# Performance work log

Measured on AMD Instinct MI355X. Metric: run time of the kernel, lower is better.

## Reference

```python
import jax, jax.numpy as jnp
import numpy as np

# B docs, N total nodes (E entities + M mentions + S sentences), R relation types, H heads
B, N, E, M, S, D, IN, R, H = 8, 224, 64, 128, 32, 256, 300, 5, 4


def setup_inputs() -> dict:
    key = jax.random.key(0)
    ks = jax.random.split(key, 24)
    p = lambda k, shp: jax.random.normal(k, shp, dtype=jnp.float32) * 0.05
    return {
        "nodes": jax.random.normal(ks[0], (B, N, IN), dtype=jnp.float32),
        "adj": (jax.random.uniform(ks[1], (B, R, N, N)) < 0.05).astype(jnp.float32),
        "mentions": jax.random.normal(ks[2], (B, M, D), dtype=jnp.float32),
        "sentences": jax.random.normal(ks[3], (B * S, D), dtype=jnp.float32),
        "Wr0": p(ks[4], (R, IN, D)), "br0": p(ks[5], (R, D)),
        "Wr1": p(ks[6], (R, D, D)), "br1": p(ks[7], (R, D)),
        "W00": p(ks[8], (IN, D)), "b00": p(ks[9], (D,)),
        "W01": p(ks[10], (D, D)), "b01": p(ks[11], (D,)),
        "Wq_h": p(ks[12], (D, D)), "Wk_h": p(ks[13], (D, D)),
        "Wv_h": p(ks[14], (D, D)), "Wo_h": p(ks[15], (D, D)),
        "Wq_t": p(ks[16], (D, D)), "Wk_t": p(ks[17], (D, D)),
        "Wv_t": p(ks[18], (D, D)), "Wo_t": p(ks[19], (D, D)),
        # entity id (local, 0..E-1) of each mention: each entity owns M/E=2 mentions
        "info_eid": (jnp.arange(B * M, dtype=jnp.int32) % E).reshape(B, M),
        # flat sentence index of each mention, within its own doc's sentence block
        "info_sid": jax.random.randint(ks[20], (B, M), 0, S, dtype=jnp.int32)
        + jnp.arange(B, dtype=jnp.int32)[:, None] * S,
    }


def _mha(key_t, value_t, query_t, mask, Wq, Wk, Wv, Wo):
    # mask: [B, P, M], True = exclude (mention does not belong to the masked entity)
    b, p, d = query_t.shape
    m = key_t.shape[1]
    dk = d // H
    Q = (query_t @ Wq).reshape(b, p, H, dk)
    K = (key_t @ Wk).reshape(b, m, H, dk)
    V = (value_t @ Wv).reshape(b, m, H, dk)
    s = jnp.einsum("bphk,bmhk->bhpm", Q, K) / jnp.sqrt(jnp.asarray(dk, Q.dtype))
    s = jnp.where(mask[:, None, :, :], jnp.asarray(-1e9, s.dtype), s)
    a = jax.nn.softmax(s, axis=-1)
    ctx = jnp.einsum("bhpm,bmhk->bphk", a, V).reshape(b, p, d)
    return ctx @ Wo


def reference(nodes, adj, mentions, sentences, Wr0, br0, Wr1, br1, W00, b00,
              W01, b01, Wq_h, Wk_h, Wv_h, Wo_h, Wq_t, Wk_t, Wv_t, Wo_t,
              info_eid, info_sid):
    # ---- RGCN_Layer: per-relation message passing, degree-normalized ----
    # denom: in-degree per node summed over relations, +1 (matches torch.sparse.sum dim=1)
    denoms = adj.sum(axis=3).sum(axis=1)[..., None] + 1.0  # [B, N, 1]

    def rgcn_layer(x, Wr, br, W0, b0):
        xW = jnp.einsum("bni,rid->brnd", x, Wr) + br[None, :, None, :]  # [B,R,N,D]
        AxW = jnp.einsum("brnm,brmd->bnd", adj, xW)  # aggregate + sum over relations
        return jax.nn.relu((AxW + x @ W0 + b0) / denoms)

    h = rgcn_layer(nodes, Wr0, br0, W00, b00)
    gcn_out = rgcn_layer(h, Wr1, br1, W01, b01)  # [B, N, D] global node reps

    # ---- Local_rep_layer: masked pairwise multi-head attention ----
    ents = gcn_out[:, :E, :]  # query='global': entities = global nodes (first E rows)
    # pair (i, j): query_1 -> entity i, query_2 -> entity j
    q1 = jnp.broadcast_to(ents[:, :, None, :], (B, E, E, D)).reshape(B, E * E, D)
    q2 = jnp.broadcast_to(ents[:, None, :, :], (B, E, E, D)).reshape(B, E * E, D)
    mention_sen_rep = sentences[info_sid]  # F.embedding(info[:,4], sentences) -> [B,M,D]
    # index_m[b, e, m] True iff mention m does NOT belong to entity e
    index_m = info_eid[:, None, :] != jnp.arange(E, dtype=info_eid.dtype)[None, :, None]
    mask_h = jnp.broadcast_to(index_m[:, :, None, :], (B, E, E, M)).reshape(B, E * E, M)
    mask_t = jnp.broadcast_to(index_m[:, None, :, :], (B, E, E, M)).reshape(B, E * E, M)
    rep_h = _mha(mention_sen_rep, mentions, q2, mask_h, Wq_h, Wk_h, Wv_h, Wo_h)
    rep_t = _mha(mention_sen_rep, mentions, q1, mask_t, Wq_t, Wk_t, Wv_t, Wo_t)
    # concatenate outputs along node axis for a single return array
    return jnp.concatenate([gcn_out, rep_h, rep_t], axis=1)  # [B, N + 2*E*E, D]
```

## Files before the change

### kernel.cpp

```cpp
#include <hip/hip_runtime.h>
#include <math.h>

#define B_ 8
#define N_ 224
#define E_ 64
#define M_ 128
#define S_ 32
#define D_ 256
#define IN_ 300
#define R_ 5
#define H_ 4
#define DK_ 64
#define OUTROWS (N_ + 2 * E_ * E_)
#define CAP_ 192
#define BN_ (B_ * N_)

typedef __attribute__((ext_vector_type(8))) short bf16x8;
typedef __attribute__((ext_vector_type(8))) unsigned short u16x8;
typedef __attribute__((ext_vector_type(4))) float f32x4;

__device__ inline short f2bf(float f) {
    union { float f; unsigned u; } x; x.f = f;
    unsigned u = x.u;
    unsigned r = (u + 0x7fffu + ((u >> 16) & 1u)) >> 16;
    return (short)r;
}
__device__ inline float bf2f(unsigned short s) {
    union { unsigned u; float f; } x; x.u = ((unsigned)s) << 16; return x.f;
}

__device__ inline void gload16(const void* g, void* l) {
    __builtin_amdgcn_global_load_lds(
        (const __attribute__((address_space(1))) unsigned int*)g,
        (__attribute__((address_space(3))) unsigned int*)l, 16, 0, 0);
}

#define PRE_PACK 1376
#define PRE_EDGE (PRE_PACK + BN_)
#define PRE_ML   (PRE_EDGE + 2)
#define CVT_N    573440
#define CVT_M    262144
#define PRE_TOT  (PRE_ML + 1072)

__global__ __launch_bounds__(256) void mega_pre(
    short* __restrict__ Wb,
    const float* Wr0, const float* W00, const float* Wr1, const float* W01,
    const float* Wkh, const float* Wkt, const float* Wvh, const float* Wvt,
    const float* Wqh, const float* Wqt, const float* Woh, const float* Wot,
    const float* __restrict__ adj, int* __restrict__ ecnt, int* __restrict__ elist,
    float* __restrict__ evals, float* __restrict__ den,
    const int* __restrict__ eid, int* __restrict__ mcnt, int* __restrict__ mlist,
    const float* __restrict__ nodes, const float* __restrict__ mentions,
    const float* __restrict__ sentences, const int* __restrict__ sid,
    short* __restrict__ nodesb, short* __restrict__ mentb, short* __restrict__ msrb) {
    __shared__ int smemi[528];
    __shared__ int wtot[4];
    __shared__ float wsum[4];
    int blk = blockIdx.x, tid = threadIdx.x;

    if (blk < PRE_PACK) {
        short (*T)[33] = (short(*)[33])smemi;
        int t = blk;
        const float* src; short* outp; int outld, klim, n0, k0;
        if (t < 480) {
            int z = t / 80, tt = t % 80;
            n0 = (tt & 7) * 32; k0 = (tt >> 3) * 32;
            outp = Wb + (size_t)z * 81920; outld = 320; klim = IN_;
            src = (z < 5) ? Wr0 + (size_t)z * IN_ * D_ : W00;
        } else if (t < 864) {
            int l = t - 480, z = l / 64, tt = l % 64;
            n0 = (tt & 7) * 32; k0 = (tt >> 3) * 32;
            outp = Wb + 491520 + (size_t)z * 65536; outld = 256; klim = 256;
            src = (z < 5) ? Wr1 + (size_t)z * D_ * D_ : W01;
        } else if (t < 992) {
            int l = t - 864, z = l / 64, tt = l % 64;
            n0 = (tt & 7) * 32; k0 = (tt >> 3) * 32;
            outp = Wb + 884736 + (size_t)z * 65536; outld = 256; klim = 256;
            src = z ? Wkt : Wkh;
        } else if (t < 1120) {
            int l = t - 992, z = l / 64, tt = l % 64;
            n0 = (tt & 7) * 32; k0 = (tt >> 3) * 32;
            outp = Wb + 1146880 + (size_t)z * 65536; outld = 256; klim = 256;
            src = z ? Wvt : Wvh;
        } else if (t < 1248) {
            int l = t - 1120, z = l / 64, tt = l % 64;
            n0 = (tt & 7) * 32; k0 = (tt >> 3) * 32;
            outp = Wb + 1409024 + (size_t)z * 65536; outld = 256; klim = 256;
            src = z ? Wqt : Wqh;
        } else {
            int l = t - 1248, z = l / 16, tt = l % 16;
            n0 = (tt & 7) * 32; k0 = (tt >> 3) * 32;
            outp = Wb + 1671168 + (size_t)z * 16384; outld = 64; klim = 64;
            int which = z >> 2, h = z & 3;
            src = (which ? Wot : Woh) + (size_t)(h * 64) * D_;
        }
        int tx = tid & 31, ty = tid >> 5;
#pragma unroll
        for (int i = 0; i < 4; ++i) {
            int k = k0 + ty + 8 * i;
            float v = (k < klim) ? src[(size_t)k * D_ + n0 + tx] : 0.f;
            T[tx][ty + 8 * i] = f2bf(v);
        }
        __syncthreads();
#pragma unroll
        for (int i = 0; i < 4; ++i) {
            int n = ty + 8 * i;
            outp[(size_t)(n0 + n) * outld + k0 + tx] = T[n][tx];
        }
    } else if (blk < PRE_EDGE) {
        int local = blk - PRE_PACK;
        int bn = (local & 7) * N_ + (local >> 3);
        int b = bn / N_, n = bn % N_;
        int lane = tid & 63, wv4 = tid >> 6;
        int idxs[5]; float vals[5];
        int cloc = 0; float sloc = 0.f;
        for (int e = tid; e < R_ * N_; e += 256) {
            int r = e / N_, m = e % N_;
            float v = adj[(((size_t)(b * R_ + r)) * N_ + n) * N_ + m];
            if (v != 0.f) { idxs[cloc] = r * BN_ + m; vals[cloc] = v; ++cloc; sloc += v; }
        }
        int v = cloc;
#pragma unroll
        for (int st = 1; st < 64; st <<= 1) {
            int o = __shfl_up(v, st, 64);
            if (lane >= st) v += o;
        }
        float fs = sloc;
#pragma unroll
        for (int st = 32; st > 0; st >>= 1) fs += __shfl_xor(fs, st, 64);
        if (lane == 63) wtot[wv4] = v;
        if (lane == 0)  wsum[wv4] = fs;
        __syncthreads();
        int woff = 0;
        for (int i = 0; i < wv4; ++i) woff += wtot[i];
        int off = woff + v - cloc;
        int total = wtot[0] + wtot[1] + wtot[2] + wtot[3];
        size_t base = (size_t)bn * CAP_;
        for (int i = 0; i < cloc; ++i) {
            int p = off + i;
            if (p < CAP_) { elist[base + p] = idxs[i]; evals[base + p] = vals[i]; }
        }
        if (tid == 0) {
            ecnt[bn] = total < CAP_ ? total : CAP_;
            den[bn] = wsum[0] + wsum[1] + wsum[2] + wsum[3] + 1.0f;
        }
    } else if (blk < PRE_ML) {
        int t = (blk - PRE_EDGE) * 256 + tid;
        if (t < B_ * E_) {
            int b = t / E_, i = t % E_;
            int c = 0;
            for (int m = 0; m < M_; ++m)
                if (eid[b * M_ + m] == i) mlist[(size_t)t * M_ + c++] = m;
            mcnt[t] = c;
        }
    } else {
        int idx = (blk - PRE_ML) * 1024 + tid * 4;
#pragma unroll
        for (int j = 0; j < 4; ++j) {
            int i = idx + j;
            if (i < CVT_N) {
                int row = i / 320, k = i % 320;
                nodesb[i] = (k < IN_) ? f2bf(nodes[(size_t)row * IN_ + k]) : (short)0;
            } else if (i < CVT_N + CVT_M) {
                int i2 = i - CVT_N;
                mentb[i2] = f2bf(mentions[i2]);
            } else {
                int i3 = i - CVT_N - CVT_M;
                int bm = i3 >> 8, d = i3 & 255;
                msrb[i3] = f2bf(sentences[(size_t)sid[bm] * D_ + d]);
            }
        }
    }
}

__global__ __launch_bounds__(256) void axw_gather(
    const short* __restrict__ xWb,
    const int* __restrict__ ecnt, const int* __restrict__ elist,
    const float* __restrict__ evals, const float* __restrict__ den,
    short* __restrict__ hb, float* __restrict__ out, long long out_bstride,
    short* __restrict__ entsb) {
    int bid = blockIdx.x;
    int bn = (bid & 7) * N_ + (bid >> 3);
    int b = bn / N_, n = bn % N_;
    int tid = threadIdx.x, wv = tid >> 6, dq = tid & 63;
    int c = ecnt[bn];
    int bno = b * N_;
    const int* lst = elist + (size_t)bn * CAP_;
    const float* vls = evals + (size_t)bn * CAP_;
    float4 acc = make_float4(0.f, 0.f, 0.f, 0.f);
#pragma unroll 2
    for (int k = wv; k < c; k += 4) {
        int rm = lst[k];
        float v = vls[k];
        ushort4 x4 = *(const ushort4*)&xWb[((size_t)(rm + bno)) * 256 + dq * 4];
        acc.x += v * bf2f(x4.x); acc.y += v * bf2f(x4.y);
        acc.z += v * bf2f(x4.z); acc.w += v * bf2f(x4.w);
    }
    __shared__ float4 red[4][64];
    red[wv][dq] = acc;
    __syncthreads();
    if (tid < 64) {
        float4 s0 = red[0][dq], s1 = red[1][dq], s2 = red[2][dq], s3 = red[3][dq];
        ushort4 t4 = *(const ushort4*)&xWb[((size_t)(5 * BN_ + bn)) * 256 + dq * 4];
        float inv = 1.f / den[bn];
        float4 o;
        o.x = fmaxf((s0.x + s1.x + s2.x + s3.x + bf2f(t4.x)) * inv, 0.f);
        o.y = fmaxf((s0.y + s1.y + s2.y + s3.y + bf2f(t4.y)) * inv, 0.f);
        o.z = fmaxf((s0.z + s1.z + s2.z + s3.z + bf2f(t4.z)) * inv, 0.f);
        o.w = fmaxf((s0.w + s1.w + s2.w + s3.w + bf2f(t4.w)) * inv, 0.f);
        if (hb) {
            ushort4 hw = { (unsigned short)f2bf(o.x), (unsigned short)f2bf(o.y),
                           (unsigned short)f2bf(o.z), (unsigned short)f2bf(o.w) };
            *(ushort4*)&hb[(size_t)bn * 256 + dq * 4] = hw;
        }
        if (out)
            *(float4*)&out[(size_t)b * out_bstride + (size_t)n * 256 + dq * 4] = o;
        if (entsb && n < E_) {
            ushort4 ew = { (unsigned short)f2bf(o.x), (unsigned short)f2bf(o.y),
                           (unsigned short)f2bf(o.z), (unsigned short)f2bf(o.w) };
            *(ushort4*)&entsb[((size_t)b * E_ + n) * 256 + dq * 4] = ew;
        }
    }
}

struct GDesc {
    const short* A; const short* Bt; short* C; const float* bias;
    int lda, ldbk, ldc, Kloop, ny;
};
struct GTable { GDesc d[14]; };

__global__ __launch_bounds__(256) void gemm_multi(GTable T) {
    GDesc g = T.d[blockIdx.z];
    if ((int)blockIdx.y >= g.ny) return;

    __shared__ short As[64 * 64];
    __shared__ short Bs[64 * 64];
    int tid = threadIdx.x;
    int lane = tid & 63, wv = tid >> 6;
    int wr = wv >> 1, wc = wv & 1;
    int fr = lane & 15;
    int so = lane >> 4;
    int row0 = blockIdx.y * 64, col0 = blockIdx.x * 64;

    int l8 = lane >> 3;
    int sl = (lane & 7) ^ l8;
    int c0 = 2 * wv, c1 = c0 + 1;
    int ra0 = row0 + 8 * c0 + l8, ra1 = row0 + 8 * c1 + l8;
    int rb0 = col0 + 8 * c0 + l8, rb1 = col0 + 8 * c1 + l8;

    f32x4 acc00 = {0.f,0.f,0.f,0.f}, acc01 = acc00, acc10 = acc00, acc11 = acc00;

    int rA0 = wr * 32 + fr, rA1 = rA0 + 16;
    int rB0 = wc * 32 + fr, rB1 = rB0 + 16;
    int sw = fr & 7;

    for (int k0 = 0; k0 < g.Kloop; k0 += 64) {
        gload16(&g.A [(size_t)ra0 * g.lda  + k0 + sl * 8], &As[c0 * 512]);
        gload16(&g.A [(size_t)ra1 * g.lda  + k0 + sl * 8], &As[c1 * 512]);
        gload16(&g.Bt[(size_t)rb0 * g.ldbk + k0 + sl * 8], &Bs[c0 * 512]);
        gload16(&g.Bt[(size_t)rb1 * g.ldbk + k0 + sl * 8], &Bs[c1 * 512]);
        __syncthreads();
#pragma unroll
        for (int ks = 0; ks < 2; ++ks) {
            int s = ks * 4 + so;
            bf16x8 a0 = *(bf16x8*)&As[rA0 * 64 + ((s ^ sw) << 3)];
            bf16x8 a1 = *(bf16x8*)&As[rA1 * 64 + ((s ^ sw) << 3)];
            bf16x8 b0 = *(bf16x8*)&Bs[rB0 * 64 + ((s ^ sw) << 3)];
            bf16x8 b1 = *(bf16x8*)&Bs[rB1 * 64 + ((s ^ sw) << 3)];
            acc00 = __builtin_amdgcn_mfma_f32_16x16x32_bf16(a0, b0, acc00, 0, 0, 0);
            acc01 = __builtin_amdgcn_mfma_f32_16x16x32_bf16(a0, b1, acc01, 0, 0, 0);
            acc10 = __builtin_amdgcn_mfma_f32_16x16x32_bf16(a1, b0, acc10, 0, 0, 0);
            acc11 = __builtin_amdgcn_mfma_f32_16x16x32_bf16(a1, b1, acc11, 0, 0, 0);
        }
        __syncthreads();
    }

    int rbase = row0 + wr * 32 + (lane >> 4) * 4;
    int cbase = col0 + wc * 32 + fr;
    f32x4 accs[2][2] = {{acc00, acc01}, {acc10, acc11}};
#pragma unroll
    for (int mi = 0; mi < 2; ++mi) {
#pragma unroll
        for (int nj = 0; nj < 2; ++nj) {
            int cc = cbase + nj * 16;
            float bval = g.bias ? g.bias[cc] : 0.f;
#pragma unroll
            for (int r = 0; r < 4; ++r) {
                int cr = rbase + mi * 16 + r;
                g.C[(size_t)cr * g.ldc + cc] = f2bf(accs[mi][nj][r] + bval);
            }
        }
    }
}

__device__ inline float dot64_bf(const short* q, const short* k) {
    float dot = 0.f;
#pragma unroll
    for (int t8 = 0; t8 < 8; ++t8) {
        u16x8 qv = *(const u16x8*)(q + t8 * 8);
        u16x8 kv = *(const u16x8*)(k + t8 * 8);
#pragma unroll
        for (int j = 0; j < 8; ++j) dot += bf2f(qv[j]) * bf2f(kv[j]);
    }
    return dot;
}

__global__ __launch_bounds__(256) void combine_kernel(
    const short* __restrict__ Qb, const short* __restrict__ Kb,
    const short* __restrict__ VWb, const int* __restrict__ cnt,
    const int* __restrict__ mlist, float* __restrict__ out) {
    int bid = blockIdx.x;
    int g = bid & 15, me = bid >> 4;
    int b = g & 7, z = g >> 3;
    const short* Q  = Qb  + (size_t)z * (B_ * E_ * D_);
    const short* K  = Kb  + (size_t)z * (B_ * M_ * D_);
    const short* VW = VWb + (size_t)z * (B_ * M_ * H_ * D_);
    int baserow = N_ + z * (E_ * E_);
    int tid = threadIdx.x;
    int dq = tid & 63;
    __shared__ float sVW[2][H_ * D_];
    __shared__ float sS[E_][H_][2];
    int c = cnt[b * E_ + me];
    const int* lst = mlist + (size_t)(b * E_ + me) * M_;

    if (c >= 1 && c <= 2) {
        for (int k = 0; k < c; ++k) {
            ushort4 v4 = *(const ushort4*)(VW + ((size_t)b * M_ + lst[k]) * (H_ * D_) + tid * 4);
            *(float4*)&sVW[k][tid * 4] =
                make_float4(bf2f(v4.x), bf2f(v4.y), bf2f(v4.z), bf2f(v4.w));
        }
        for (int e = tid; e < E_ * H_ * 2; e += 256) {
            int k = e & 1, hh = (e >> 1) & 3, ql = e >> 3;
            if (k < c) {
                const short* Qrow = Q + ((size_t)b * E_ + ql) * D_ + hh * DK_;
                const short* Krow = K + ((size_t)b * M_ + lst[k]) * D_ + hh * DK_;
                sS[ql][hh][k] = dot64_bf(Qrow, Krow) * 0.125f;
            }
        }
        __syncthreads();
        {
            int hh = tid & 3, ql = tid >> 2;
            float mx = sS[ql][hh][0];
            for (int k = 1; k < c; ++k) mx = fmaxf(mx, sS[ql][hh][k]);
            float w[2]; float sm = 0.f;
            for (int k = 0; k < c; ++k) { w[k] = __expf(sS[ql][hh][k] - mx); sm += w[k]; }
            float inv = 1.f / sm;
            for (int k = 0; k < c; ++k) sS[ql][hh][k] = w[k] * inv;
        }
        __syncthreads();
        for (int qq = tid >> 6; qq < E_; qq += 4) {
            float4 acc = make_float4(0.f, 0.f, 0.f, 0.f);
#pragma unroll
            for (int hh = 0; hh < H_; ++hh)
                for (int k = 0; k < c; ++k) {
                    float w = sS[qq][hh][k];
                    float4 v = *(const float4*)&sVW[k][hh * D_ + dq * 4];
                    acc.x += w * v.x; acc.y += w * v.y; acc.z += w * v.z; acc.w += w * v.w;
                }
            int row = z ? (qq * E_ + me) : (me * E_ + qq);
            *(float4*)&out[((size_t)b * OUTROWS + baserow + row) * D_ + dq * 4] = acc;
        }
    } else if (c == 0) {
        float s = 0.f;
        for (int m = 0; m < M_; ++m)
            for (int hh = 0; hh < H_; ++hh)
                s += bf2f((unsigned short)VW[((size_t)b * M_ + m) * (H_ * D_) + hh * D_ + tid]);
        sVW[0][tid] = s * (1.0f / M_);
        __syncthreads();
        for (int qq = tid >> 6; qq < E_; qq += 4) {
            float4 v = *(const float4*)&sVW[0][dq * 4];
            int row = z ? (qq * E_ + me) : (me * E_ + qq);
            *(float4*)&out[((size_t)b * OUTROWS + baserow + row) * D_ + dq * 4] = v;
        }
    } else {
        {
            int hh = tid & 3, ql = tid >> 2;
            const short* Qrow = Q + ((size_t)b * E_ + ql) * D_ + hh * DK_;
            float mx = -1e30f;
            for (int k = 0; k < c; ++k) {
                const short* Krow = K + ((size_t)b * M_ + lst[k]) * D_ + hh * DK_;
                mx = fmaxf(mx, dot64_bf(Qrow, Krow) * 0.125f);
            }
            float sm = 0.f;
            for (int k = 0; k < c; ++k) {
                const short* Krow = K + ((size_t)b * M_ + lst[k]) * D_ + hh * DK_;
                sm += __expf(dot64_bf(Qrow, Krow) * 0.125f - mx);
            }
            sS[ql][hh][0] = mx;
            sS[ql][hh][1] = sm;
        }
        __syncthreads();
        for (int qq = tid >> 6; qq < E_; qq += 4) {
            float4 acc = make_float4(0.f, 0.f, 0.f, 0.f);
            for (int hh = 0; hh < H_; ++hh) {
                float mx = sS[qq][hh][0], inv = 1.f / sS[qq][hh][1];
                const short* Qrow = Q + ((size_t)b * E_ + qq) * D_ + hh * DK_;
                for (int k = 0; k < c; ++k) {
                    const short* Krow = K + ((size_t)b * M_ + lst[k]) * D_ + hh * DK_;
                    float w = __expf(dot64_bf(Qrow, Krow) * 0.125f - mx) * inv;
                    ushort4 v4 = *(const ushort4*)(VW + ((size_t)b * M_ + lst[k]) * (H_ * D_) + hh * D_ + dq * 4);
                    acc.x += w * bf2f(v4.x); acc.y += w * bf2f(v4.y);
                    acc.z += w * bf2f(v4.z); acc.w += w * bf2f(v4.w);
                }
            }
            int row = z ? (qq * E_ + me) : (me * E_ + qq);
            *(float4*)&out[((size_t)b * OUTROWS + baserow + row) * D_ + dq * 4] = acc;
        }
    }
}

extern "C" void kernel_launch(void* const* d_in, const int* in_sizes, int n_in,
                              void* d_out, int out_size, void* d_ws, size_t ws_size,
                              hipStream_t stream) {
    const float* nodes     = (const float*)d_in[0];
    const float* adj       = (const float*)d_in[1];
    const float* mentions  = (const float*)d_in[2];
    const float* sentences = (const float*)d_in[3];
    const float* Wr0 = (const float*)d_in[4];
    const float* br0 = (const float*)d_in[5];
    const float* Wr1 = (const float*)d_in[6];
    const float* br1 = (const float*)d_in[7];
    const float* W00 = (const float*)d_in[8];
    const float* b00 = (const float*)d_in[9];
    const float* W01 = (const float*)d_in[10];
    const float* b01 = (const float*)d_in[11];
    const float* Wq_h = (const float*)d_in[12];
    const float* Wk_h = (const float*)d_in[13];
    const float* Wv_h = (const float*)d_in[14];
    const float* Wo_h = (const float*)d_in[15];
    const float* Wq_t = (const float*)d_in[16];
    const float* Wk_t = (const float*)d_in[17];
    const float* Wv_t = (const float*)d_in[18];
    const float* Wo_t = (const float*)d_in[19];
    const int* info_eid = (const int*)d_in[20];
    const int* info_sid = (const int*)d_in[21];
    float* out  = (float*)d_out;
    float* pool = (float*)d_ws;

    short* xWb   = (short*)pool;
    short* hb    = (short*)(pool + 1376256);
    short* entsb = (short*)(pool + 1605632);
    short* KVb   = (short*)(pool + 1671168);
    short* nodesb= (short*)(pool + 2195456);
    short* msrb  = (short*)(pool + 2482176);
    short* mentb = (short*)(pool + 2613248);
    short* Wb    = (short*)(pool + 2744320);
    int*   elist = (int*)(pool + 3645440);
    float* evals = pool + 3989504;
    int*   ecnt  = (int*)(pool + 4333568);
    float* den   = pool + 4335360;
    int*   mcnt  = (int*)(pool + 4337152);
    int*   mlist = (int*)(pool + 4337664);
    short* VWb   = (short*)(pool + 4403200);
    short* Qb    = (short*)(pool + 5451776);

    short* W1t = Wb;
    short* W2t = Wb + 491520;
    short* WKt = Wb + 884736;
    short* WVt = Wb + 1146880;
    short* WQt = Wb + 1409024;
    short* WOt = Wb + 1671168;

    mega_pre<<<PRE_TOT, 256, 0, stream>>>(
        Wb, Wr0, W00, Wr1, W01, Wk_h, Wk_t, Wv_h, Wv_t, Wq_h, Wq_t, Wo_h, Wo_t,
        adj, ecnt, elist, evals, den, info_eid, mcnt, mlist,
        nodes, mentions, sentences, info_sid, nodesb, mentb, msrb);

    {
        GTable T = {};
        for (int z = 0; z < 6; ++z)
            T.d[z] = { nodesb, W1t + z * 81920, xWb + (size_t)z * BN_ * D_,
                       (z < 5) ? br0 + z * D_ : b00, 320, 320, D_, 320, 28 };
        for (int zp = 0; zp < 4; ++zp) {
            int half = zp >> 1, wt = zp & 1;
            T.d[6 + zp] = { msrb + half * 262144, (half ? WVt : WKt) + wt * 65536,
                            KVb + half * 524288 + wt * 262144,
                            nullptr, D_, D_, D_, D_, 16 };
        }
        gemm_multi<<<dim3(4, 28, 10), 256, 0, stream>>>(T);
    }
    axw_gather<<<BN_, 256, 0, stream>>>(xWb, ecnt, elist, evals, den,
                                        hb, nullptr, 0, nullptr);
    {
        GTable T = {};
        for (int z = 0; z < 6; ++z)
            T.d[z] = { hb, W2t + z * 65536, xWb + (size_t)z * BN_ * D_,
                       (z < 5) ? br1 + z * D_ : b01, D_, D_, D_, D_, 28 };
        for (int zp = 0; zp < 8; ++zp) {
            int which = zp >> 2, hh = zp & 3;
            T.d[6 + zp] = { KVb + 524288 + which * 262144 + hh * DK_,
                            WOt + which * 65536 + hh * 16384,
                            VWb + (size_t)which * (B_ * M_ * H_ * D_) + hh * D_,
                            nullptr, D_, DK_, H_ * D_, DK_, 16 };
        }
        gemm_multi<<<dim3(4, 28, 14), 256, 0, stream>>>(T);
    }
    axw_gather<<<BN_, 256, 0, stream>>>(xWb, ecnt, elist, evals, den,
                                        nullptr, out, (long long)OUTROWS * D_, entsb);
    {
        GTable T = {};
        for (int which = 0; which < 2; ++which)
            T.d[which] = { entsb, WQt + which * 65536, Qb + which * 131072,
                           nullptr, D_, D_, D_, D_, 8 };
        gemm_multi<<<dim3(4, 8, 2), 256, 0, stream>>>(T);
    }
    combine_kernel<<<E_ * B_ * 2, 256, 0, stream>>>(Qb, KVb, VWb, mcnt, mlist, out);
}
```

Baseline: 91.74 us.

## Fold query projection into keys to drop the Q GEMM launch

Result: slower. 146.2 us (+59.3%).

```diff
diff --git a/kernel.cpp b/kernel.cpp
--- a/kernel.cpp
+++ b/kernel.cpp
@@ -40,7 +40,9 @@
 #define PRE_ML   (PRE_EDGE + 2)
 #define CVT_N    573440
 #define CVT_M    262144
-#define PRE_TOT  (PRE_ML + 1072)
+#define CVT_S    262144
+#define CVT_Q    131072
+#define PRE_TOT  (PRE_ML + 1200)
 
 __global__ __launch_bounds__(256) void mega_pre(
     short* __restrict__ Wb,
@@ -52,7 +54,8 @@
     const int* __restrict__ eid, int* __restrict__ mcnt, int* __restrict__ mlist,
     const float* __restrict__ nodes, const float* __restrict__ mentions,
     const float* __restrict__ sentences, const int* __restrict__ sid,
-    short* __restrict__ nodesb, short* __restrict__ mentb, short* __restrict__ msrb) {
+    short* __restrict__ nodesb, short* __restrict__ mentb, short* __restrict__ msrb,
+    short* __restrict__ WQs) {
     __shared__ int smemi[528];
     __shared__ int wtot[4];
     __shared__ float wsum[4];
@@ -164,10 +167,13 @@
             } else if (i < CVT_N + CVT_M) {
                 int i2 = i - CVT_N;
                 mentb[i2] = f2bf(mentions[i2]);
-            } else {
+            } else if (i < CVT_N + CVT_M + CVT_S) {
                 int i3 = i - CVT_N - CVT_M;
                 int bm = i3 >> 8, d = i3 & 255;
                 msrb[i3] = f2bf(sentences[(size_t)sid[bm] * D_ + d]);
+            } else {
+                int i4 = i - CVT_N - CVT_M - CVT_S;
+                WQs[i4] = f2bf(i4 >= 65536 ? Wqt[i4 - 65536] : Wqh[i4]);
             }
         }
     }
@@ -177,8 +183,7 @@
     const short* __restrict__ xWb,
     const int* __restrict__ ecnt, const int* __restrict__ elist,
     const float* __restrict__ evals, const float* __restrict__ den,
-    short* __restrict__ hb, float* __restrict__ out, long long out_bstride,
-    short* __restrict__ entsb) {
+    short* __restrict__ hb, float* __restrict__ out, long long out_bstride) {
     int bid = blockIdx.x;
     int bn = (bid & 7) * N_ + (bid >> 3);
     int b = bn / N_, n = bn % N_;
@@ -215,11 +220,6 @@
         }
         if (out)
             *(float4*)&out[(size_t)b * out_bstride + (size_t)n * 256 + dq * 4] = o;
-        if (entsb && n < E_) {
-            ushort4 ew = { (unsigned short)f2bf(o.x), (unsigned short)f2bf(o.y),
-                           (unsigned short)f2bf(o.z), (unsigned short)f2bf(o.w) };
-            *(ushort4*)&entsb[((size_t)b * E_ + n) * 256 + dq * 4] = ew;
-        }
     }
 }
 
@@ -227,7 +227,7 @@
     const short* A; const short* Bt; short* C; const float* bias;
     int lda, ldbk, ldc, Kloop, ny;
 };
-struct GTable { GDesc d[14]; };
+struct GTable { GDesc d[22]; };
 
 __global__ __launch_bounds__(256) void gemm_multi(GTable T) {
     GDesc g = T.d[blockIdx.z];
@@ -293,28 +293,28 @@
     }
 }
 
-__device__ inline float dot64_bf(const short* q, const short* k) {
+__device__ inline float dot256_f_bf(const float* e, const short* kq) {
     float dot = 0.f;
 #pragma unroll
-    for (int t8 = 0; t8 < 8; ++t8) {
-        u16x8 qv = *(const u16x8*)(q + t8 * 8);
-        u16x8 kv = *(const u16x8*)(k + t8 * 8);
-#pragma unroll
-        for (int j = 0; j < 8; ++j) dot += bf2f(qv[j]) * bf2f(kv[j]);
+    for (int t8 = 0; t8 < 32; ++t8) {
+        u16x8 kv = *(const u16x8*)(kq + t8 * 8);
+        float4 e0 = *(const float4*)(e + t8 * 8);
+        float4 e1 = *(const float4*)(e + t8 * 8 + 4);
+        dot += e0.x * bf2f(kv[0]) + e0.y * bf2f(kv[1]) + e0.z * bf2f(kv[2]) + e0.w * bf2f(kv[3])
+             + e1.x * bf2f(kv[4]) + e1.y * bf2f(kv[5]) + e1.z * bf2f(kv[6]) + e1.w * bf2f(kv[7]);
     }
     return dot;
 }
 
 __global__ __launch_bounds__(256) void combine_kernel(
-    const short* __restrict__ Qb, const short* __restrict__ Kb,
-    const short* __restrict__ VWb, const int* __restrict__ cnt,
-    const int* __restrict__ mlist, float* __restrict__ out) {
+    const short* __restrict__ KQb, const short* __restrict__ VWb,
+    const int* __restrict__ cnt, const int* __restrict__ mlist,
+    float* __restrict__ out) {
     int bid = blockIdx.x;
     int g = bid & 15, me = bid >> 4;
     int b = g & 7, z = g >> 3;
-    const short* Q  = Qb  + (size_t)z * (B_ * E_ * D_);
-    const short* K  = Kb  + (size_t)z * (B_ * M_ * D_);
     const short* VW = VWb + (size_t)z * (B_ * M_ * H_ * D_);
+    const float* ents = out + (size_t)b * OUTROWS * D_;
     int baserow = N_ + z * (E_ * E_);
     int tid = threadIdx.x;
     int dq = tid & 63;
@@ -332,9 +332,9 @@
         for (int e = tid; e < E_ * H_ * 2; e += 256) {
             int k = e & 1, hh = (e >> 1) & 3, ql = e >> 3;
             if (k < c) {
-                const short* Qrow = Q + ((size_t)b * E_ + ql) * D_ + hh * DK_;
-                const short* Krow = K + ((size_t)b * M_ + lst[k]) * D_ + hh * DK_;
-                sS[ql][hh][k] = dot64_bf(Qrow, Krow) * 0.125f;
+                const short* KQrow = KQb + ((size_t)(z * 4 + hh)) * (B_ * M_ * D_)
+                                         + ((size_t)b * M_ + lst[k]) * D_;
+                sS[ql][hh][k] = dot256_f_bf(ents + (size_t)ql * D_, KQrow) * 0.125f;
             }
         }
         __syncthreads();
@@ -375,16 +375,18 @@
     } else {
         {
             int hh = tid & 3, ql = tid >> 2;
-            const short* Qrow = Q + ((size_t)b * E_ + ql) * D_ + hh * DK_;
+            const float* erow = ents + (size_t)ql * D_;
             float mx = -1e30f;
             for (int k = 0; k < c; ++k) {
-                const short* Krow = K + ((size_t)b * M_ + lst[k]) * D_ + hh * DK_;
-                mx = fmaxf(mx, dot64_bf(Qrow, Krow) * 0.125f);
+                const short* KQrow = KQb + ((size_t)(z * 4 + hh)) * (B_ * M_ * D_)
+                                         + ((size_t)b * M_ + lst[k]) * D_;
+                mx = fmaxf(mx, dot256_f_bf(erow, KQrow) * 0.125f);
             }
             float sm = 0.f;
             for (int k = 0; k < c; ++k) {
-                const short* Krow = K + ((size_t)b * M_ + lst[k]) * D_ + hh * DK_;
-                sm += __expf(dot64_bf(Qrow, Krow) * 0.125f - mx);
+                const short* KQrow = KQb + ((size_t)(z * 4 + hh)) * (B_ * M_ * D_)
+                                         + ((size_t)b * M_ + lst[k]) * D_;
+                sm += __expf(dot256_f_bf(erow, KQrow) * 0.125f - mx);
             }
             sS[ql][hh][0] = mx;
             sS[ql][hh][1] = sm;
@@ -392,12 +394,13 @@
         __syncthreads();
         for (int qq = tid >> 6; qq < E_; qq += 4) {
             float4 acc = make_float4(0.f, 0.f, 0.f, 0.f);
+            const float* erow = ents + (size_t)qq * D_;
             for (int hh = 0; hh < H_; ++hh) {
                 float mx = sS[qq][hh][0], inv = 1.f / sS[qq][hh][1];
-                const short* Qrow = Q + ((size_t)b * E_ + qq) * D_ + hh * DK_;
                 for (int k = 0; k < c; ++k) {
-                    const short* Krow = K + ((size_t)b * M_ + lst[k]) * D_ + hh * DK_;
-                    float w = __expf(dot64_bf(Qrow, Krow) * 0.125f - mx) * inv;
+                    const short* KQrow = KQb + ((size_t)(z * 4 + hh)) * (B_ * M_ * D_)
+                                             + ((size_t)b * M_ + lst[k]) * D_;
+                    float w = __expf(dot256_f_bf(erow, KQrow) * 0.125f - mx) * inv;
                     ushort4 v4 = *(const ushort4*)(VW + ((size_t)b * M_ + lst[k]) * (H_ * D_) + hh * D_ + dq * 4);
                     acc.x += w * bf2f(v4.x); acc.y += w * bf2f(v4.y);
                     acc.z += w * bf2f(v4.z); acc.w += w * bf2f(v4.w);
@@ -439,7 +442,6 @@
 
     short* xWb   = (short*)pool;
     short* hb    = (short*)(pool + 1376256);
-    short* entsb = (short*)(pool + 1605632);
     short* KVb   = (short*)(pool + 1671168);
     short* nodesb= (short*)(pool + 2195456);
     short* msrb  = (short*)(pool + 2482176);
@@ -452,19 +454,19 @@
     int*   mcnt  = (int*)(pool + 4337152);
     int*   mlist = (int*)(pool + 4337664);
     short* VWb   = (short*)(pool + 4403200);
-    short* Qb    = (short*)(pool + 5451776);
+    short* KQb   = (short*)(pool + 5451776);
+    short* WQs   = (short*)(pool + 6500352);
 
     short* W1t = Wb;
     short* W2t = Wb + 491520;
     short* WKt = Wb + 884736;
     short* WVt = Wb + 1146880;
-    short* WQt = Wb + 1409024;
     short* WOt = Wb + 1671168;
 
     mega_pre<<<PRE_TOT, 256, 0, stream>>>(
         Wb, Wr0, W00, Wr1, W01, Wk_h, Wk_t, Wv_h, Wv_t, Wq_h, Wq_t, Wo_h, Wo_t,
         adj, ecnt, elist, evals, den, info_eid, mcnt, mlist,
-        nodes, mentions, sentences, info_sid, nodesb, mentb, msrb);
+        nodes, mentions, sentences, info_sid, nodesb, mentb, msrb, WQs);
 
     {
         GTable T = {};
@@ -480,7 +482,7 @@
         gemm_multi<<<dim3(4, 28, 10), 256, 0, stream>>>(T);
     }
     axw_gather<<<BN_, 256, 0, stream>>>(xWb, ecnt, elist, evals, den,
-                                        hb, nullptr, 0, nullptr);
+                                        hb, nullptr, 0);
     {
         GTable T = {};
         for (int z = 0; z < 6; ++z)
@@ -493,16 +495,16 @@
                             VWb + (size_t)which * (B_ * M_ * H_ * D_) + hh * D_,
                             nullptr, D_, DK_, H_ * D_, DK_, 16 };
         }
-        gemm_multi<<<dim3(4, 28, 14), 256, 0, stream>>>(T);
+        for (int zp = 0; zp < 8; ++zp) {
+            int which = zp >> 2, hh = zp & 3;
+            T.d[14 + zp] = { KVb + which * 262144 + hh * DK_,
+                             WQs + which * 65536 + hh * DK_,
+                             KQb + (size_t)(which * 4 + hh) * (B_ * M_ * D_),
+                             nullptr, D_, D_, D_, DK_, 16 };
+        }
+        gemm_multi<<<dim3(4, 28, 22), 256, 0, stream>>>(T);
     }
     axw_gather<<<BN_, 256, 0, stream>>>(xWb, ecnt, elist, evals, den,
-                                        nullptr, out, (long long)OUTROWS * D_, entsb);
-    {
-        GTable T = {};
-        for (int which = 0; which < 2; ++which)
-            T.d[which] = { entsb, WQt + which * 65536, Qb + which * 131072,
-                           nullptr, D_, D_, D_, D_, 8 };
-        gemm_multi<<<dim3(4, 8, 2), 256, 0, stream>>>(T);
-    }
-    combine_kernel<<<E_ * B_ * 2, 256, 0, stream>>>(Qb, KVb, VWb, mcnt, mlist, out);
-}
+                                        nullptr, out, (long long)OUTROWS * D_);
+    combine_kernel<<<E_ * B_ * 2, 256, 0, stream>>>(KQb, VWb, mcnt, mlist, out);
+}
```
